# Kernel tuning notes

Measured on AMD Instinct MI355X. Metric: run time of the kernel, lower is better.

Reference implementation:

```python
import jax, jax.numpy as jnp
import numpy as np

NFPS = 10

def setup_inputs() -> dict:
    key = jax.random.key(0)
    k1, k2, k3, k4 = jax.random.split(key, 4)
    B, D_IN, H, D_OUT = 131072, 2 * NFPS * 3, 256, NFPS * 3 * 12
    x = jax.random.normal(k1, (B, D_IN), dtype=jnp.float32)
    centres = jax.random.normal(k2, (H, D_IN), dtype=jnp.float32)
    sigmas = jax.random.uniform(k3, (H,), dtype=jnp.float32)
    W2 = jax.random.normal(k4, (D_OUT, H), dtype=jnp.float32) * (1.0 / np.sqrt(H))
    return {"x": x, "centres": centres, "sigmas": sigmas, "W2": W2}

def reference(x, centres, sigmas, W2):
    # RBF layer: distances = ||x - c|| * sigma; gaussian: exp(-distances^2)
    x2 = jnp.sum(x * x, axis=-1, keepdims=True)            # [B,1]
    c2 = jnp.sum(centres * centres, axis=-1)               # [H]
    xc = jnp.einsum('bd,hd->bh', x, centres)               # [B,H]
    d2 = jnp.maximum(x2 + c2[None, :] - 2.0 * xc, 0.0)     # squared distance, clamp fp noise
    phi = jnp.exp(-(sigmas[None, :] ** 2) * d2)            # [B,H]
    out = jnp.einsum('bh,oh->bo', phi, W2)                 # [B, nFPs*3*12]
    B = x.shape[0]
    out = out.reshape(B, NFPS, 12, 3).transpose(0, 1, 3, 2).reshape(B, 3 * NFPS, 12)
    return out
```

## Files before the change

kernel.cpp:

```cpp
#include <hip/hip_runtime.h>

#define THREADS 512
#define DIN 60
#define HN 256
#define DOUT 360

typedef __attribute__((ext_vector_type(8))) short short8;
typedef __attribute__((ext_vector_type(16))) float f32x16;
typedef __attribute__((ext_vector_type(4))) float f32x4;
typedef __attribute__((ext_vector_type(2))) float f32x2;
typedef __attribute__((ext_vector_type(4))) unsigned int u32x4;

#define WS_CBF   0
#define WS_CN    32768
#define WS_W2    34816

__device__ __forceinline__ short bf16_bits(float f) {
    union { float f; unsigned u; } v; v.f = f;
    unsigned r = (v.u + 0x7FFFu + ((v.u >> 16) & 1u)) >> 16;
    return (short)(unsigned short)r;
}

__device__ __forceinline__ unsigned pk_bf16(float a, float b) {
    unsigned r;
    asm("v_cvt_pk_bf16_f32 %0, %1, %2" : "=v"(r) : "v"(a), "v"(b));
    return r;
}

__device__ __forceinline__ void gload16(const void* g, void* lds) {
    __builtin_amdgcn_global_load_lds(
        (const __attribute__((address_space(1))) unsigned int*)(uintptr_t)g,
        (__attribute__((address_space(3))) unsigned int*)(unsigned int)(uintptr_t)lds,
        16, 0, 0);
}

__global__ void prep(const float* __restrict__ centres, const float* __restrict__ sigmas,
                     const float* __restrict__ W2, short* __restrict__ ws)
{
    int t = blockIdx.x * 256 + threadIdx.x;
    if (t < 12288) {
        int row = t >> 5, pc = t & 31;
        int c = pc ^ (row & 31);
        short8 v = {0,0,0,0,0,0,0,0};
        if (row < DOUT) {
            int rr = row / 12, jj = row % 12;
            int f = rr / 3, kk = rr % 3;
            int o = f * 36 + jj * 3 + kk;
            const float* src = W2 + o * HN + c * 8;
            #pragma unroll
            for (int i = 0; i < 8; ++i) v[i] = bf16_bits(src[i]);
        }
        *(short8*)(ws + (WS_W2 / 2) + t * 8) = v;
    } else if (t < 14336) {
        int j = t - 12288;
        int row = j >> 3, p = j & 7;
        int c = p ^ (row & 7);
        short8 v = {0,0,0,0,0,0,0,0};
        #pragma unroll
        for (int i = 0; i < 8; ++i) {
            int k = c * 8 + i;
            if (k < DIN) v[i] = bf16_bits(centres[row * DIN + k]);
        }
        *(short8*)(ws + (WS_CBF / 2) + j * 8) = v;
    } else if (t < 14592) {
        int i = t - 14336;
        const float* cr = centres + i * DIN;
        float s = 0.f;
        #pragma unroll
        for (int d = 0; d < DIN; ++d) s = fmaf(cr[d], cr[d], s);
        float sg = sigmas[i];
        float ns2 = -sg * sg * 1.44269504088896340736f;
        f32x2 v; v[0] = ns2; v[1] = ns2 * s;
        *(f32x2*)(ws + (WS_CN / 2) + i * 4) = v;
    }
}

__global__ __launch_bounds__(THREADS, 2)
void rbf_main(const float* __restrict__ x, const short* __restrict__ ws,
              float* __restrict__ out)
{
    __shared__ short8 w2h[6144];
    __shared__ short8 cbf[2048];
    __shared__ f32x2  cnsl[HN];

    const int tid   = threadIdx.x;
    const int w     = tid >> 6;
    const int lane  = tid & 63;
    const int l31   = lane & 31;
    const int hi    = lane >> 5;
    const int f     = blockIdx.x & 1;
    const int sbase = blockIdx.x >> 1;

    #pragma unroll
    for (int i = 0; i < 12; ++i)
        gload16(ws + (WS_W2 / 2) + ((size_t)f * 6144 + i * THREADS + tid) * 8,
                (char*)w2h + (i * THREADS + tid) * 16);
    #pragma unroll
    for (int i = 0; i < 4; ++i)
        gload16(ws + (WS_CBF / 2) + (i * THREADS + tid) * 8, (char*)cbf + (i * THREADS + tid) * 16);
    if (tid < 128)
        gload16(ws + (WS_CN / 2) + tid * 8, (char*)cnsl + tid * 16);

    int rbase = sbase * 1024 + w * 32;
    f32x4 xa[4][2];
    {
        const float* xr = x + (size_t)(rbase + l31) * DIN;
        #pragma unroll
        for (int kt = 0; kt < 4; ++kt) {
            int k0 = kt * 16 + hi * 8;
            xa[kt][0] = *(const f32x4*)(xr + k0);
            xa[kt][1] = (k0 + 4 < DIN) ? *(const f32x4*)(xr + k0 + 4) : (f32x4){0.f,0.f,0.f,0.f};
        }
    }
    float p2 = 0.f;
    #pragma unroll
    for (int kt = 0; kt < 4; ++kt)
        #pragma unroll
        for (int h = 0; h < 2; ++h)
            #pragma unroll
            for (int i = 0; i < 4; ++i) p2 = fmaf(xa[kt][h][i], xa[kt][h][i], p2);
    float x2v = p2 + __shfl_xor(p2, 32);
    short8 xb[4];
    #pragma unroll
    for (int kt = 0; kt < 4; ++kt) {
        union { u32x4 u; short8 s; } a;
        a.u[0] = pk_bf16(xa[kt][0][0], xa[kt][0][1]);
        a.u[1] = pk_bf16(xa[kt][0][2], xa[kt][0][3]);
        a.u[2] = pk_bf16(xa[kt][1][0], xa[kt][1][1]);
        a.u[3] = pk_bf16(xa[kt][1][2], xa[kt][1][3]);
        xb[kt] = a.s;
    }

    __syncthreads();

    for (int it = 0; it < 4; ++it) {
        if (it < 3) {
            const float* xr = x + (size_t)(rbase + 256 + l31) * DIN;
            #pragma unroll
            for (int kt = 0; kt < 4; ++kt) {
                int k0 = kt * 16 + hi * 8;
                xa[kt][0] = *(const f32x4*)(xr + k0);
                xa[kt][1] = (k0 + 4 < DIN) ? *(const f32x4*)(xr + k0 + 4) : (f32x4){0.f,0.f,0.f,0.f};
            }
        }

        unsigned pw[32][2];
        #pragma unroll
        for (int h2 = 0; h2 < 2; ++h2) {
            f32x16 a1[4];
            #pragma unroll
            for (int nt = 0; nt < 4; ++nt) a1[nt] = (f32x16){};
            __builtin_amdgcn_s_setprio(1);
            #pragma unroll
            for (int nt = 0; nt < 4; ++nt) {
                int row = (h2 * 4 + nt) * 32 + l31;
                #pragma unroll
                for (int kt = 0; kt < 4; ++kt) {
                    short8 cf = cbf[row * 8 + ((kt * 2 + hi) ^ (row & 7))];
                    a1[nt] = __builtin_amdgcn_mfma_f32_32x32x16_bf16(cf, xb[kt], a1[nt], 0, 0, 0);
                }
            }
            __builtin_amdgcn_s_setprio(0);
            #pragma unroll
            for (int nt = 0; nt < 4; ++nt) {
                int ntg = h2 * 4 + nt;
                float ph[16];
                #pragma unroll
                for (int r = 0; r < 16; ++r) {
                    int h = ntg * 32 + (r & 3) + 8 * (r >> 2) + 4 * hi;
                    f32x2 cn = cnsl[h];
                    float t = fmaf(-2.f, a1[nt][r], x2v);
                    ph[r] = exp2f(fminf(fmaf(cn[0], t, cn[1]), 0.f));
                }
                #pragma unroll
                for (int q = 0; q < 4; ++q) {
                    pw[ntg * 4 + q][0] = pk_bf16(ph[4 * q + 0], ph[4 * q + 1]);
                    pw[ntg * 4 + q][1] = pk_bf16(ph[4 * q + 2], ph[4 * q + 3]);
                }
            }
        }

        float x2n = 0.f;
        if (it < 3) {
            float q2 = 0.f;
            #pragma unroll
            for (int kt = 0; kt < 4; ++kt)
                #pragma unroll
                for (int h = 0; h < 2; ++h)
                    #pragma unroll
                    for (int i = 0; i < 4; ++i) q2 = fmaf(xa[kt][h][i], xa[kt][h][i], q2);
            x2n = q2 + __shfl_xor(q2, 32);
            #pragma unroll
            for (int kt = 0; kt < 4; ++kt) {
                union { u32x4 u; short8 s; } a;
                a.u[0] = pk_bf16(xa[kt][0][0], xa[kt][0][1]);
                a.u[1] = pk_bf16(xa[kt][0][2], xa[kt][0][3]);
                a.u[2] = pk_bf16(xa[kt][1][0], xa[kt][1][1]);
                a.u[3] = pk_bf16(xa[kt][1][2], xa[kt][1][3]);
                xb[kt] = a.s;
            }
        }

        f32x16 a2[6];
        #pragma unroll
        for (int nt = 0; nt < 6; ++nt) a2[nt] = (f32x16){};
        #pragma unroll
        for (int kt = 0; kt < 16; ++kt) {
            const int b = kt * 2;
            int A0 = __shfl((int)pw[b][0],     l31);
            int A1 = __shfl((int)pw[b][1],     l31);
            int C0 = __shfl((int)pw[b + 1][0], l31);
            int C1 = __shfl((int)pw[b + 1][1], l31);
            int B0 = __shfl((int)pw[b][0],     l31 + 32);
            int B1 = __shfl((int)pw[b][1],     l31 + 32);
            int D0 = __shfl((int)pw[b + 1][0], l31 + 32);
            int D1 = __shfl((int)pw[b + 1][1], l31 + 32);
            union { u32x4 u; short8 s; } bf;
            bf.u[0] = (unsigned)(hi ? C0 : A0);
            bf.u[1] = (unsigned)(hi ? C1 : A1);
            bf.u[2] = (unsigned)(hi ? D0 : B0);
            bf.u[3] = (unsigned)(hi ? D1 : B1);

            __builtin_amdgcn_s_setprio(1);
            #pragma unroll
            for (int nt = 0; nt < 6; ++nt) {
                int lrow = nt * 32 + l31;
                short8 wf = w2h[lrow * 32 + ((kt * 2 + hi) ^ l31)];
                a2[nt] = __builtin_amdgcn_mfma_f32_32x32x16_bf16(wf, bf.s, a2[nt], 0, 0, 0);
            }
            __builtin_amdgcn_s_setprio(0);
        }

        {
            float* op = out + (size_t)(rbase + l31) * DOUT;
            #pragma unroll
            for (int nt = 0; nt < 6; ++nt) {
                #pragma unroll
                for (int q = 0; q < 4; ++q) {
                    int col = f * 192 + nt * 32 + q * 8 + hi * 4;
                    if (col < DOUT) {
                        f32x4 v;
                        v[0] = a2[nt][4 * q + 0]; v[1] = a2[nt][4 * q + 1];
                        v[2] = a2[nt][4 * q + 2]; v[3] = a2[nt][4 * q + 3];
                        *(f32x4*)(op + col) = v;
                    }
                }
            }
        }

        x2v = x2n;
        rbase += 256;
    }
}

extern "C" void kernel_launch(void* const* d_in, const int* in_sizes, int n_in,
                              void* d_out, int out_size, void* d_ws, size_t ws_size,
                              hipStream_t stream) {
    const float* x       = (const float*)d_in[0];
    const float* centres = (const float*)d_in[1];
    const float* sigmas  = (const float*)d_in[2];
    const float* W2      = (const float*)d_in[3];
    float* out = (float*)d_out;
    short* ws  = (short*)d_ws;
    prep<<<dim3(57), dim3(256), 0, stream>>>(centres, sigmas, W2, ws);
    rbf_main<<<dim3(256), dim3(THREADS), 0, stream>>>(x, ws, out);
}
```

Measured before the change: 71.99 us.

## Fold squared norms into MFMA, stream W2 from global, compute all outputs per block

Folds ||c||^2 and ||x||^2 into the first MFMA through padding slots: centres carry -0.5*c2 split into hi/lo bf16 parts, and x carries a 1 and its x2 hi/lo. The exponent then becomes a single multiply by a per-hidden scale. W2 is no longer staged in LDS. Each block now covers all 360 outputs in two passes, reading W2 fragments directly from global/L2 with double-buffered register prefetch, and writes results with nontemporal stores. This cuts LDS use and the duplicated first GEMM across the output halves, but adds global reads of W2 per wave and some bf16 precision risk in the folded norms.

Measured after the change: 140.5 us. 1.95x slower.

```diff
diff --git a/kernel.cpp b/kernel.cpp
--- a/kernel.cpp
+++ b/kernel.cpp
@@ -39,14 +39,13 @@
 {
     int t = blockIdx.x * 256 + threadIdx.x;
     if (t < 12288) {
-        int row = t >> 5, pc = t & 31;
-        int c = pc ^ (row & 31);
+        int kc = t / 384, row = t % 384;
         short8 v = {0,0,0,0,0,0,0,0};
         if (row < DOUT) {
             int rr = row / 12, jj = row % 12;
-            int f = rr / 3, kk = rr % 3;
-            int o = f * 36 + jj * 3 + kk;
-            const float* src = W2 + o * HN + c * 8;
+            int fcl = rr / 3, kk = rr % 3;
+            int o = fcl * 36 + jj * 3 + kk;
+            const float* src = W2 + o * HN + kc * 8;
             #pragma unroll
             for (int i = 0; i < 8; ++i) v[i] = bf16_bits(src[i]);
         }
@@ -56,22 +55,32 @@
         int row = j >> 3, p = j & 7;
         int c = p ^ (row & 7);
         short8 v = {0,0,0,0,0,0,0,0};
-        #pragma unroll
-        for (int i = 0; i < 8; ++i) {
-            int k = c * 8 + i;
-            if (k < DIN) v[i] = bf16_bits(centres[row * DIN + k]);
+        const float* cr = centres + row * DIN;
+        if (c < 7) {
+            #pragma unroll
+            for (int i = 0; i < 8; ++i) {
+                int k = c * 8 + i;
+                if (k < DIN) v[i] = bf16_bits(cr[k]);
+            }
+        } else {
+            #pragma unroll
+            for (int i = 0; i < 4; ++i) v[i] = bf16_bits(cr[56 + i]);
+            float c2 = 0.f;
+            #pragma unroll
+            for (int d = 0; d < DIN; ++d) c2 = fmaf(cr[d], cr[d], c2);
+            union { unsigned u; float f; } hb;
+            hb.u = ((unsigned)(unsigned short)bf16_bits(c2)) << 16;
+            float c2lo = c2 - hb.f;
+            v[4] = bf16_bits(-0.5f * hb.f);
+            v[5] = bf16_bits(-0.5f * c2lo);
+            v[6] = bf16_bits(-0.5f);
+            v[7] = bf16_bits(-0.5f);
         }
         *(short8*)(ws + (WS_CBF / 2) + j * 8) = v;
     } else if (t < 14592) {
         int i = t - 14336;
-        const float* cr = centres + i * DIN;
-        float s = 0.f;
-        #pragma unroll
-        for (int d = 0; d < DIN; ++d) s = fmaf(cr[d], cr[d], s);
         float sg = sigmas[i];
-        float ns2 = -sg * sg * 1.44269504088896340736f;
-        f32x2 v; v[0] = ns2; v[1] = ns2 * s;
-        *(f32x2*)(ws + (WS_CN / 2) + i * 4) = v;
+        ((float*)ws)[WS_CN / 4 + i] = 2.f * sg * sg * 1.44269504088896340736f;
     }
 }
 
@@ -79,29 +88,23 @@
 void rbf_main(const float* __restrict__ x, const short* __restrict__ ws,
               float* __restrict__ out)
 {
-    __shared__ short8 w2h[6144];
     __shared__ short8 cbf[2048];
-    __shared__ f32x2  cnsl[HN];
-
-    const int tid   = threadIdx.x;
-    const int w     = tid >> 6;
-    const int lane  = tid & 63;
-    const int l31   = lane & 31;
-    const int hi    = lane >> 5;
-    const int f     = blockIdx.x & 1;
-    const int sbase = blockIdx.x >> 1;
-
-    #pragma unroll
-    for (int i = 0; i < 12; ++i)
-        gload16(ws + (WS_W2 / 2) + ((size_t)f * 6144 + i * THREADS + tid) * 8,
-                (char*)w2h + (i * THREADS + tid) * 16);
+    __shared__ __attribute__((aligned(16))) float nsl[HN];
+
+    const int tid  = threadIdx.x;
+    const int w    = tid >> 6;
+    const int lane = tid & 63;
+    const int l31  = lane & 31;
+    const int hi   = lane >> 5;
+    const short* wbase = ws + (WS_W2 / 2);
+
     #pragma unroll
     for (int i = 0; i < 4; ++i)
         gload16(ws + (WS_CBF / 2) + (i * THREADS + tid) * 8, (char*)cbf + (i * THREADS + tid) * 16);
-    if (tid < 128)
-        gload16(ws + (WS_CN / 2) + tid * 8, (char*)cnsl + tid * 16);
-
-    int rbase = sbase * 1024 + w * 32;
+    if (tid < 64)
+        gload16(ws + (WS_CN / 2) + tid * 8, (char*)nsl + tid * 16);
+
+    int rbase = blockIdx.x * 512 + w * 32;
     f32x4 xa[4][2];
     {
         const float* xr = x + (size_t)(rbase + l31) * DIN;
@@ -112,29 +115,38 @@
             xa[kt][1] = (k0 + 4 < DIN) ? *(const f32x4*)(xr + k0 + 4) : (f32x4){0.f,0.f,0.f,0.f};
         }
     }
-    float p2 = 0.f;
+    short8 xb[4];
+    {
+        float p2 = 0.f;
+        #pragma unroll
+        for (int kt = 0; kt < 4; ++kt)
+            #pragma unroll
+            for (int h = 0; h < 2; ++h)
+                #pragma unroll
+                for (int i = 0; i < 4; ++i) p2 = fmaf(xa[kt][h][i], xa[kt][h][i], p2);
+        float x2v = p2 + __shfl_xor(p2, 32);
+        union { unsigned u; float f; } hb; hb.u = pk_bf16(x2v, 0.f) << 16;
+        float x2lo = x2v - hb.f;
+        #pragma unroll
+        for (int kt = 0; kt < 4; ++kt) {
+            union { u32x4 u; short8 s; } a;
+            a.u[0] = pk_bf16(xa[kt][0][0], xa[kt][0][1]);
+            a.u[1] = pk_bf16(xa[kt][0][2], xa[kt][0][3]);
+            a.u[2] = pk_bf16(xa[kt][1][0], xa[kt][1][1]);
+            a.u[3] = pk_bf16(xa[kt][1][2], xa[kt][1][3]);
+            if (kt == 3) {
+                a.u[2] = hi ? 0x3F803F80u : a.u[2];
+                a.u[3] = hi ? pk_bf16(hb.f, x2lo) : a.u[3];
+            }
+            xb[kt] = a.s;
+        }
+    }
+
+    __syncthreads();
+
     #pragma unroll
-    for (int kt = 0; kt < 4; ++kt)
-        #pragma unroll
-        for (int h = 0; h < 2; ++h)
-            #pragma unroll
-            for (int i = 0; i < 4; ++i) p2 = fmaf(xa[kt][h][i], xa[kt][h][i], p2);
-    float x2v = p2 + __shfl_xor(p2, 32);
-    short8 xb[4];
-    #pragma unroll
-    for (int kt = 0; kt < 4; ++kt) {
-        union { u32x4 u; short8 s; } a;
-        a.u[0] = pk_bf16(xa[kt][0][0], xa[kt][0][1]);
-        a.u[1] = pk_bf16(xa[kt][0][2], xa[kt][0][3]);
-        a.u[2] = pk_bf16(xa[kt][1][0], xa[kt][1][1]);
-        a.u[3] = pk_bf16(xa[kt][1][2], xa[kt][1][3]);
-        xb[kt] = a.s;
-    }
-
-    __syncthreads();
-
-    for (int it = 0; it < 4; ++it) {
-        if (it < 3) {
+    for (int it = 0; it < 2; ++it) {
+        if (it == 0) {
             const float* xr = x + (size_t)(rbase + 256 + l31) * DIN;
             #pragma unroll
             for (int kt = 0; kt < 4; ++kt) {
@@ -164,24 +176,21 @@
             #pragma unroll
             for (int nt = 0; nt < 4; ++nt) {
                 int ntg = h2 * 4 + nt;
-                float ph[16];
-                #pragma unroll
-                for (int r = 0; r < 16; ++r) {
-                    int h = ntg * 32 + (r & 3) + 8 * (r >> 2) + 4 * hi;
-                    f32x2 cn = cnsl[h];
-                    float t = fmaf(-2.f, a1[nt][r], x2v);
-                    ph[r] = exp2f(fminf(fmaf(cn[0], t, cn[1]), 0.f));
-                }
                 #pragma unroll
                 for (int q = 0; q < 4; ++q) {
-                    pw[ntg * 4 + q][0] = pk_bf16(ph[4 * q + 0], ph[4 * q + 1]);
-                    pw[ntg * 4 + q][1] = pk_bf16(ph[4 * q + 2], ph[4 * q + 3]);
-                }
-            }
-        }
-
-        float x2n = 0.f;
-        if (it < 3) {
+                    f32x4 ns4 = *(const f32x4*)(nsl + ntg * 32 + 8 * q + 4 * hi);
+                    float ph[4];
+                    #pragma unroll
+                    for (int j = 0; j < 4; ++j)
+                        ph[j] = exp2f(fminf(ns4[j] * a1[nt][4 * q + j], 0.f));
+                    pw[ntg * 4 + q][0] = pk_bf16(ph[0], ph[1]);
+                    pw[ntg * 4 + q][1] = pk_bf16(ph[2], ph[3]);
+                }
+            }
+        }
+
+        short8 xbn[4];
+        if (it == 0) {
             float q2 = 0.f;
             #pragma unroll
             for (int kt = 0; kt < 4; ++kt)
@@ -189,7 +198,9 @@
                 for (int h = 0; h < 2; ++h)
                     #pragma unroll
                     for (int i = 0; i < 4; ++i) q2 = fmaf(xa[kt][h][i], xa[kt][h][i], q2);
-            x2n = q2 + __shfl_xor(q2, 32);
+            float x2n = q2 + __shfl_xor(q2, 32);
+            union { unsigned u; float f; } hb; hb.u = pk_bf16(x2n, 0.f) << 16;
+            float x2lo = x2n - hb.f;
             #pragma unroll
             for (int kt = 0; kt < 4; ++kt) {
                 union { u32x4 u; short8 s; } a;
@@ -197,58 +208,74 @@
                 a.u[1] = pk_bf16(xa[kt][0][2], xa[kt][0][3]);
                 a.u[2] = pk_bf16(xa[kt][1][0], xa[kt][1][1]);
                 a.u[3] = pk_bf16(xa[kt][1][2], xa[kt][1][3]);
-                xb[kt] = a.s;
-            }
-        }
-
-        f32x16 a2[6];
-        #pragma unroll
-        for (int nt = 0; nt < 6; ++nt) a2[nt] = (f32x16){};
-        #pragma unroll
-        for (int kt = 0; kt < 16; ++kt) {
-            const int b = kt * 2;
-            int A0 = __shfl((int)pw[b][0],     l31);
-            int A1 = __shfl((int)pw[b][1],     l31);
-            int C0 = __shfl((int)pw[b + 1][0], l31);
-            int C1 = __shfl((int)pw[b + 1][1], l31);
-            int B0 = __shfl((int)pw[b][0],     l31 + 32);
-            int B1 = __shfl((int)pw[b][1],     l31 + 32);
-            int D0 = __shfl((int)pw[b + 1][0], l31 + 32);
-            int D1 = __shfl((int)pw[b + 1][1], l31 + 32);
-            union { u32x4 u; short8 s; } bf;
-            bf.u[0] = (unsigned)(hi ? C0 : A0);
-            bf.u[1] = (unsigned)(hi ? C1 : A1);
-            bf.u[2] = (unsigned)(hi ? D0 : B0);
-            bf.u[3] = (unsigned)(hi ? D1 : B1);
-
-            __builtin_amdgcn_s_setprio(1);
+                if (kt == 3) {
+                    a.u[2] = hi ? 0x3F803F80u : a.u[2];
+                    a.u[3] = hi ? pk_bf16(hb.f, x2lo) : a.u[3];
+                }
+                xbn[kt] = a.s;
+            }
+        }
+
+        #pragma unroll
+        for (int pass = 0; pass < 2; ++pass) {
+            f32x16 a2[6];
+            #pragma unroll
+            for (int nt = 0; nt < 6; ++nt) a2[nt] = (f32x16){};
+            short8 gf[2][6];
+            #pragma unroll
+            for (int nt = 0; nt < 6; ++nt)
+                gf[0][nt] = *(const short8*)(wbase + ((size_t)hi * 384 + pass * 192 + nt * 32 + l31) * 8);
+
+            #pragma unroll
+            for (int kt = 0; kt < 16; ++kt) {
+                if (kt < 15) {
+                    #pragma unroll
+                    for (int nt = 0; nt < 6; ++nt)
+                        gf[(kt + 1) & 1][nt] = *(const short8*)(wbase +
+                            ((size_t)((kt + 1) * 2 + hi) * 384 + pass * 192 + nt * 32 + l31) * 8);
+                }
+                const int b = kt * 2;
+                int A0 = __shfl((int)pw[b][0],     l31);
+                int A1 = __shfl((int)pw[b][1],     l31);
+                int C0 = __shfl((int)pw[b + 1][0], l31);
+                int C1 = __shfl((int)pw[b + 1][1], l31);
+                int B0 = __shfl((int)pw[b][0],     l31 + 32);
+                int B1 = __shfl((int)pw[b][1],     l31 + 32);
+                int D0 = __shfl((int)pw[b + 1][0], l31 + 32);
+                int D1 = __shfl((int)pw[b + 1][1], l31 + 32);
+                union { u32x4 u; short8 s; } bf;
+                bf.u[0] = (unsigned)(hi ? C0 : A0);
+                bf.u[1] = (unsigned)(hi ? C1 : A1);
+                bf.u[2] = (unsigned)(hi ? D0 : B0);
+                bf.u[3] = (unsigned)(hi ? D1 : B1);
+
+                __builtin_amdgcn_s_setprio(1);
+                #pragma unroll
+                for (int nt = 0; nt < 6; ++nt)
+                    a2[nt] = __builtin_amdgcn_mfma_f32_32x32x16_bf16(gf[kt & 1][nt], bf.s, a2[nt], 0, 0, 0);
+                __builtin_amdgcn_s_setprio(0);
+            }
+
+            float* op = out + (size_t)(rbase + l31) * DOUT;
             #pragma unroll
             for (int nt = 0; nt < 6; ++nt) {
-                int lrow = nt * 32 + l31;
-                short8 wf = w2h[lrow * 32 + ((kt * 2 + hi) ^ l31)];
-                a2[nt] = __builtin_amdgcn_mfma_f32_32x32x16_bf16(wf, bf.s, a2[nt], 0, 0, 0);
-            }
-            __builtin_amdgcn_s_setprio(0);
-        }
-
-        {
-            float* op = out + (size_t)(rbase + l31) * DOUT;
-            #pragma unroll
-            for (int nt = 0; nt < 6; ++nt) {
                 #pragma unroll
                 for (int q = 0; q < 4; ++q) {
-                    int col = f * 192 + nt * 32 + q * 8 + hi * 4;
-                    if (col < DOUT) {
+                    int cb = pass * 192 + nt * 32 + q * 8;
+                    if (cb < DOUT) {
                         f32x4 v;
                         v[0] = a2[nt][4 * q + 0]; v[1] = a2[nt][4 * q + 1];
                         v[2] = a2[nt][4 * q + 2]; v[3] = a2[nt][4 * q + 3];
-                        *(f32x4*)(op + col) = v;
+                        __builtin_nontemporal_store(v, (f32x4*)(op + cb + hi * 4));
                     }
                 }
             }
         }
 
-        x2v = x2n;
+        if (it == 0) {
+            #pragma unroll
+            for (int kt = 0; kt < 4; ++kt) xb[kt] = xbn[kt];
+        }
         rbase += 256;
     }
 }
```
